# Performance work log

Measured on AMD Instinct MI355X. Metric: run time of the kernel, lower is better.

Reference implementation:

```python
import jax, jax.numpy as jnp
from jax import lax
import numpy as np

T, B, I, H, F, KEEP = 1000, 512, 64, 64, 128, 5
ALPHA = 20.0 / 100.0  # dt / tau


def setup_inputs() -> dict:
    key = jax.random.key(0)
    ks = jax.random.split(key, 9)
    s = 1.0 / np.sqrt(H)
    return {
        "x": jax.random.normal(ks[0], (T, B, I), jnp.float32),
        "h0": jnp.zeros((B, H), jnp.float32),
        "W_in": jax.random.normal(ks[1], (H, I), jnp.float32) * s,
        "b_in": jax.random.normal(ks[2], (H,), jnp.float32) * s,
        "W_hh": jax.random.normal(ks[3], (H, H), jnp.float32) * s,
        "b_hh": jax.random.normal(ks[4], (H,), jnp.float32) * s,
        "W1": jax.random.normal(ks[5], (F, KEEP * H), jnp.float32) / np.sqrt(KEEP * H),
        "b1": jax.random.normal(ks[6], (F,), jnp.float32) * 0.01,
        "W2": jax.random.normal(ks[7], (H, F), jnp.float32) / np.sqrt(F),
        "b2": jax.random.normal(ks[8], (H,), jnp.float32) * 0.01,
    }


def reference(x, h0, W_in, b_in, W_hh, b_hh, W1, b1, W2, b2):
    # CT-RNN with leaky integration; feedback via MLP on the last 5 hiddens
    # once 5 steps have accumulated. KC = 0.5*I, so the feedback mix is
    # h = 0.5*h_obs + 0.5*h_mlp.
    Tn, Bn, _ = x.shape
    Hn = h0.shape[1]
    buf0 = jnp.zeros((KEEP, Bn, Hn), x.dtype)  # oldest-first ring of hiddens

    def step(carry, inp):
        h, buf = carry
        xt, i = inp
        h_obs = jax.nn.relu(xt @ W_in.T + b_in + h @ W_hh.T + b_hh)
        h_obs = h * (1.0 - ALPHA) + h_obs * ALPHA
        # mlp feedback on concat of last 5 hiddens (oldest..newest) -> [B, 5H]
        mlp_in = buf.transpose(1, 0, 2).reshape(Bn, KEEP * Hn)
        h_mlp = jax.nn.relu(mlp_in @ W1.T + b1) @ W2.T + b2
        h_new = jnp.where(i >= KEEP, 0.5 * h_obs + 0.5 * h_mlp, h_obs)
        buf = jnp.concatenate([buf[1:], h_new[None]], axis=0)
        return (h_new, buf), h_new

    (hT, _), out = lax.scan(step, (h0, buf0), (x, jnp.arange(Tn)))
    return out, hT
```

## Files before the change

kernel.cpp:

```cpp
#include <hip/hip_runtime.h>

typedef short bf16x8 __attribute__((ext_vector_type(8)));
typedef float f32x4  __attribute__((ext_vector_type(4)));

#define TSTEPS 1000
#define BATCH  512
#define HID    64
#define INPD   64
#define FEAT   128
#define KEEP   5
#define KH     320
#define ALPHA  0.2f
#define BB     2
#define NBLK   (BATCH/BB)
#define NTHR   512

#define MFMA(a,b,c) __builtin_amdgcn_mfma_f32_16x16x32_bf16(a, b, c, 0, 0, 0)

template<int P> struct IC { static constexpr int v = P; };

__device__ __forceinline__ void barrier_fast() {
  asm volatile("s_waitcnt lgkmcnt(0)" ::: "memory");
  __builtin_amdgcn_s_barrier();
  asm volatile("" ::: "memory");
}

__device__ __forceinline__ f32x4 fold2(f32x4 v) {
  f32x4 r;
  r.x = v.x + __shfl_xor(v.x, 2);
  r.y = v.y + __shfl_xor(v.y, 2);
  r.z = v.z + __shfl_xor(v.z, 2);
  r.w = v.w + __shfl_xor(v.w, 2);
  return r;
}

__device__ __forceinline__ void pack4(float x0, float x1, float x2, float x3,
                                      unsigned &h0, unsigned &h1,
                                      unsigned &l0, unsigned &l1) {
  unsigned a0 = __float_as_uint(x0), a1 = __float_as_uint(x1);
  unsigned a2 = __float_as_uint(x2), a3 = __float_as_uint(x3);
  h0 = __builtin_amdgcn_perm(a1, a0, 0x07060302u);
  h1 = __builtin_amdgcn_perm(a3, a2, 0x07060302u);
  float r0 = x0 - __uint_as_float(a0 & 0xFFFF0000u);
  float r1 = x1 - __uint_as_float(a1 & 0xFFFF0000u);
  float r2 = x2 - __uint_as_float(a2 & 0xFFFF0000u);
  float r3 = x3 - __uint_as_float(a3 & 0xFFFF0000u);
  asm("v_cvt_pk_bf16_f32 %0, %1, %2" : "=v"(l0) : "v"(r0), "v"(r1));
  asm("v_cvt_pk_bf16_f32 %0, %1, %2" : "=v"(l1) : "v"(r2), "v"(r3));
}

__device__ __forceinline__ void pack_frag(float4 v0, float4 v1, bf16x8 &hi, bf16x8 &lo) {
  int4 h4, l4;
  pack4(v0.x, v0.y, v0.z, v0.w, (unsigned&)h4.x, (unsigned&)h4.y, (unsigned&)l4.x, (unsigned&)l4.y);
  pack4(v1.x, v1.y, v1.z, v1.w, (unsigned&)h4.z, (unsigned&)h4.w, (unsigned&)l4.z, (unsigned&)l4.w);
  hi = __builtin_bit_cast(bf16x8, h4);
  lo = __builtin_bit_cast(bf16x8, l4);
}

__device__ __forceinline__ void load_wfrag(const float* p, bf16x8 &hi, bf16x8 &lo) {
  float4 v0 = *(const float4*)p;
  float4 v1 = *(const float4*)(p + 4);
  pack_frag(v0, v1, hi, lo);
}

__global__ __launch_bounds__(NTHR, 2) void seq_kernel(
    const float* __restrict__ x,    float* __restrict__ io,
    const float* __restrict__ h0g,
    const float* __restrict__ W_in, const float* __restrict__ b_in,
    const float* __restrict__ W_hh, const float* __restrict__ b_hh,
    const float* __restrict__ W1,   const float* __restrict__ b1,
    const float* __restrict__ W2,   const float* __restrict__ b2) {

  __shared__ __align__(16) short B1lds[1024];
  __shared__ __align__(16) short a_s[512];
  __shared__ __align__(16) float xin_s[2][128];

  const int tid  = threadIdx.x;
  const int w    = tid >> 6;
  const int lane = tid & 63;
  const int q15  = lane & 15;
  const int g    = lane >> 4;
  const int b0   = blockIdx.x * BB;
  const bool gA  = (w < 4);
  const int r0c  = 16*(w & 3) + 4*g;
  const int f0   = 16*w + 4*g;
  const int c01  = q15 & 1;

  const int aWH = (w>>1)*128 + (2*(w&1) + (g>>1))*32 + q15*8 + 4*(g&1);
  const int aRD = g*32 + (q15 & 3)*8;
  const int bWH = ((w&3)>>1)*512 + ((2*(w&3) + (g>>1)) & 3)*128 + q15*8 + 4*(g&1);
  const int bRD = g*128 + q15*8;

  const f32x4 vz = {0.f, 0.f, 0.f, 0.f};
  const bf16x8 z8 = {0,0,0,0,0,0,0,0};

  bf16x8 w1h[10], w1l[10];
#pragma unroll
  for (int jt = 0; jt < 10; ++jt)
    load_wfrag(W1 + (size_t)(16*w + q15)*KH + jt*32 + 8*g, w1h[jt], w1l[jt]);

  bf16x8 wxh[6], wxl[6];
#pragma unroll
  for (int i = 0; i < 6; ++i) { wxh[i] = z8; wxl[i] = z8; }
  f32x4 biasv = vz, b2r = vz;
  f32x4 b1r = *(const f32x4*)(b1 + f0);
  if (gA) {
#pragma unroll
    for (int kt = 0; kt < 2; ++kt)
      load_wfrag(W_hh + (size_t)(16*w + q15)*HID + kt*32 + 8*g, wxh[kt], wxl[kt]);
#pragma unroll
    for (int kt = 0; kt < 4; ++kt)
      load_wfrag(W2 + (size_t)(16*w + q15)*FEAT + kt*32 + 8*g, wxh[2+kt], wxl[2+kt]);
    b2r = *(const f32x4*)(b2 + r0c);
  } else {
#pragma unroll
    for (int kt = 0; kt < 2; ++kt)
      load_wfrag(W_in + (size_t)(16*(w-4) + q15)*INPD + kt*32 + 8*g, wxh[kt], wxl[kt]);
    biasv = *(const f32x4*)(b_in + r0c) + *(const f32x4*)(b_hh + r0c);
  }

  for (int i = tid; i < 512; i += NTHR) ((unsigned*)B1lds)[i] = 0u;
  __syncthreads();

  f32x4 hprev = vz;
  float4 xc0, xc1, xc2, xc3;
  if (gA) {
    if (q15 < 2) {
      hprev = *(const f32x4*)(h0g + (size_t)(b0 + q15)*HID + r0c);
      unsigned n0, n1, n2, n3;
      pack4(hprev.x, hprev.y, hprev.z, hprev.w, n0, n1, n2, n3);
      *(uint2*)&B1lds[bWH]      = make_uint2(n0, n1);
      *(uint2*)&B1lds[bWH + 16] = make_uint2(n2, n3);
    }
  } else {
    const float* xp = x + (size_t)(b0 + c01)*INPD + 8*g;
    float4 v0 = *(const float4*)xp;        float4 v1 = *(const float4*)(xp + 4);
    float4 v2 = *(const float4*)(xp + 32); float4 v3 = *(const float4*)(xp + 36);
    bf16x8 th0, tl0, th1, tl1;
    pack_frag(v0, v1, th0, tl0);
    pack_frag(v2, v3, th1, tl1);
    bf16x8 f0b = (q15 & 2) ? tl0 : th0;
    bf16x8 f1b = (q15 & 2) ? tl1 : th1;
    f32x4 aH = vz, aL = vz;
    aH = MFMA(wxh[0], f0b, aH); aH = MFMA(wxh[1], f1b, aH);
    aL = MFMA(wxl[0], f0b, aL); aL = MFMA(wxl[1], f1b, aL);
    f32x4 xi = fold2(aH + aL) + biasv;
    if (q15 < 2) *(f32x4*)&xin_s[0][q15*64 + r0c] = xi;
    const float* xq = x + (size_t)1*BATCH*INPD + (size_t)(b0 + c01)*INPD + 8*g;
    xc0 = *(const float4*)xq;        xc1 = *(const float4*)(xq + 4);
    xc2 = *(const float4*)(xq + 32); xc3 = *(const float4*)(xq + 36);
  }

  bf16x8 rb[KEEP][2];
#pragma unroll
  for (int s = 0; s < KEEP; ++s) { rb[s][0] = z8; rb[s][1] = z8; }
  __syncthreads();

  int t5 = 0;
  auto step = [&](auto pc) {
    constexpr int ph = decltype(pc)::v;
    constexpr int sN = (ph + 4) % 5;
    const int t = t5 + ph;

    float4 xn0, xn1, xn2, xn3;
    if (!gA) {
      int tn = t + 2; if (tn > TSTEPS-1) tn = TSTEPS-1;
      const float* xp = x + (size_t)tn*BATCH*INPD + (size_t)(b0 + c01)*INPD + 8*g;
      xn0 = *(const float4*)xp;        xn1 = *(const float4*)(xp + 4);
      xn2 = *(const float4*)(xp + 32); xn3 = *(const float4*)(xp + 36);
    }

    rb[sN][0] = *(const bf16x8*)&B1lds[bRD];
    rb[sN][1] = *(const bf16x8*)&B1lds[bRD + 512];

    f32x4 aH = vz, aL = vz;
#pragma unroll
    for (int e = 1; e <= 5; ++e) {
      const int s = (sN + e) % 5;
      const int r = ((s - ph) % 5 + 5) % 5;
#pragma unroll
      for (int q = 0; q < 2; ++q) {
        const int jt = 2*r + q;
        aH = MFMA(w1h[jt], rb[s][q], aH);
        aL = MFMA(w1l[jt], rb[s][q], aL);
      }
    }
    {
      f32x4 apre = fold2(aH + aL) + b1r;
      f32x4 av = __builtin_elementwise_max(apre, vz);
      unsigned p0, p1, p2, p3;
      pack4(av.x, av.y, av.z, av.w, p0, p1, p2, p3);
      if (q15 < 2) {
        *(uint2*)&a_s[aWH]      = make_uint2(p0, p1);
        *(uint2*)&a_s[aWH + 16] = make_uint2(p2, p3);
      }
    }

    if (!gA) {
      bf16x8 th0, tl0, th1, tl1;
      pack_frag(xc0, xc1, th0, tl0);
      pack_frag(xc2, xc3, th1, tl1);
      bf16x8 f0b = (q15 & 2) ? tl0 : th0;
      bf16x8 f1b = (q15 & 2) ? tl1 : th1;
      f32x4 xH = vz, xL = vz;
      xH = MFMA(wxh[0], f0b, xH); xH = MFMA(wxh[1], f1b, xH);
      xL = MFMA(wxl[0], f0b, xL); xL = MFMA(wxl[1], f1b, xL);
      f32x4 xi = fold2(xH + xL) + biasv;
      if (q15 < 2) *(f32x4*)&xin_s[(t + 1) & 1][q15*64 + r0c] = xi;
      xc0 = xn0; xc1 = xn1; xc2 = xn2; xc3 = xn3;
    }
    barrier_fast();

    if (gA) {
      bf16x8 af0 = *(const bf16x8*)&a_s[aRD +   0];
      bf16x8 af1 = *(const bf16x8*)&a_s[aRD + 128];
      bf16x8 af2 = *(const bf16x8*)&a_s[aRD + 256];
      bf16x8 af3 = *(const bf16x8*)&a_s[aRD + 384];
      f32x4 xinv = *(const f32x4*)&xin_s[t & 1][(q15 & 1)*64 + r0c];
      f32x4 rH = vz, rL = vz;
      rH = MFMA(wxh[0], rb[sN][0], rH); rH = MFMA(wxh[1], rb[sN][1], rH);
      rL = MFMA(wxl[0], rb[sN][0], rL); rL = MFMA(wxl[1], rb[sN][1], rL);
      f32x4 mH = vz, mL = vz;
      mH = MFMA(wxh[2], af0, mH); mL = MFMA(wxl[2], af0, mL);
      mH = MFMA(wxh[3], af1, mH); mL = MFMA(wxl[3], af1, mL);
      mH = MFMA(wxh[4], af2, mH); mL = MFMA(wxl[4], af2, mL);
      mH = MFMA(wxh[5], af3, mH); mL = MFMA(wxl[5], af3, mL);
      f32x4 pre = fold2(rH + rL) + xinv;
      f32x4 rl_ = __builtin_elementwise_max(pre, vz);
      f32x4 hobs = hprev * (1.f - ALPHA) + rl_ * ALPHA;
      f32x4 hm = fold2(mH + mL) + b2r;
      f32x4 hn = (t >= KEEP) ? (hobs + hm) * 0.5f : hobs;
      if (q15 < 2) {
        *(f32x4*)(io + (size_t)t*BATCH*HID + (size_t)(b0 + q15)*HID + r0c) = hn;
        if (t == TSTEPS-1)
          *(f32x4*)(io + (size_t)TSTEPS*BATCH*HID + (size_t)(b0 + q15)*HID + r0c) = hn;
        unsigned n0, n1, n2, n3;
        pack4(hn.x, hn.y, hn.z, hn.w, n0, n1, n2, n3);
        *(uint2*)&B1lds[bWH]      = make_uint2(n0, n1);
        *(uint2*)&B1lds[bWH + 16] = make_uint2(n2, n3);
      }
      hprev = hn;
    }
    barrier_fast();
  };

  for (t5 = 0; t5 < TSTEPS; t5 += 5) {
    step(IC<0>{});
    step(IC<1>{});
    step(IC<2>{});
    step(IC<3>{});
    step(IC<4>{});
  }
}

extern "C" void kernel_launch(void* const* d_in, const int* in_sizes, int n_in,
                              void* d_out, int out_size, void* d_ws, size_t ws_size,
                              hipStream_t stream) {
  (void)in_sizes; (void)n_in; (void)out_size; (void)d_ws; (void)ws_size;
  const float* x    = (const float*)d_in[0];
  const float* h0   = (const float*)d_in[1];
  const float* W_in = (const float*)d_in[2];
  const float* b_in = (const float*)d_in[3];
  const float* W_hh = (const float*)d_in[4];
  const float* b_hh = (const float*)d_in[5];
  const float* W1   = (const float*)d_in[6];
  const float* b1   = (const float*)d_in[7];
  const float* W2   = (const float*)d_in[8];
  const float* b2   = (const float*)d_in[9];
  float* out = (float*)d_out;

  seq_kernel<<<NBLK, NTHR, 0, stream>>>(x, out, h0, W_in, b_in, W_hh, b_hh, W1, b1, W2, b2);
}
```

Before: 1.159 ms.

## Precompute older-history MLP partial sums in previous step off the critical path

```diff
diff --git a/kernel.cpp b/kernel.cpp
--- a/kernel.cpp
+++ b/kernel.cpp
@@ -141,10 +141,10 @@
     pack_frag(v2, v3, th1, tl1);
     bf16x8 f0b = (q15 & 2) ? tl0 : th0;
     bf16x8 f1b = (q15 & 2) ? tl1 : th1;
-    f32x4 aH = vz, aL = vz;
-    aH = MFMA(wxh[0], f0b, aH); aH = MFMA(wxh[1], f1b, aH);
-    aL = MFMA(wxl[0], f0b, aL); aL = MFMA(wxl[1], f1b, aL);
-    f32x4 xi = fold2(aH + aL) + biasv;
+    f32x4 aHx = vz, aLx = vz;
+    aHx = MFMA(wxh[0], f0b, aHx); aHx = MFMA(wxh[1], f1b, aHx);
+    aLx = MFMA(wxl[0], f0b, aLx); aLx = MFMA(wxl[1], f1b, aLx);
+    f32x4 xi = fold2(aHx + aLx) + biasv;
     if (q15 < 2) *(f32x4*)&xin_s[0][q15*64 + r0c] = xi;
     const float* xq = x + (size_t)1*BATCH*INPD + (size_t)(b0 + c01)*INPD + 8*g;
     xc0 = *(const float4*)xq;        xc1 = *(const float4*)(xq + 4);
@@ -154,6 +154,8 @@
   bf16x8 rb[KEEP][2];
 #pragma unroll
   for (int s = 0; s < KEEP; ++s) { rb[s][0] = z8; rb[s][1] = z8; }
+
+  f32x4 aH = vz, aL = vz;
   __syncthreads();
 
   int t5 = 0;
@@ -162,29 +164,13 @@
     constexpr int sN = (ph + 4) % 5;
     const int t = t5 + ph;
 
-    float4 xn0, xn1, xn2, xn3;
-    if (!gA) {
-      int tn = t + 2; if (tn > TSTEPS-1) tn = TSTEPS-1;
-      const float* xp = x + (size_t)tn*BATCH*INPD + (size_t)(b0 + c01)*INPD + 8*g;
-      xn0 = *(const float4*)xp;        xn1 = *(const float4*)(xp + 4);
-      xn2 = *(const float4*)(xp + 32); xn3 = *(const float4*)(xp + 36);
-    }
-
     rb[sN][0] = *(const bf16x8*)&B1lds[bRD];
     rb[sN][1] = *(const bf16x8*)&B1lds[bRD + 512];
 
-    f32x4 aH = vz, aL = vz;
-#pragma unroll
-    for (int e = 1; e <= 5; ++e) {
-      const int s = (sN + e) % 5;
-      const int r = ((s - ph) % 5 + 5) % 5;
-#pragma unroll
-      for (int q = 0; q < 2; ++q) {
-        const int jt = 2*r + q;
-        aH = MFMA(w1h[jt], rb[s][q], aH);
-        aL = MFMA(w1l[jt], rb[s][q], aL);
-      }
-    }
+    aH = MFMA(w1h[8], rb[sN][0], aH);
+    aL = MFMA(w1l[8], rb[sN][0], aL);
+    aH = MFMA(w1h[9], rb[sN][1], aH);
+    aL = MFMA(w1l[9], rb[sN][1], aL);
     {
       f32x4 apre = fold2(aH + aL) + b1r;
       f32x4 av = __builtin_elementwise_max(apre, vz);
@@ -195,28 +181,23 @@
         *(uint2*)&a_s[aWH + 16] = make_uint2(p2, p3);
       }
     }
-
-    if (!gA) {
-      bf16x8 th0, tl0, th1, tl1;
-      pack_frag(xc0, xc1, th0, tl0);
-      pack_frag(xc2, xc3, th1, tl1);
-      bf16x8 f0b = (q15 & 2) ? tl0 : th0;
-      bf16x8 f1b = (q15 & 2) ? tl1 : th1;
-      f32x4 xH = vz, xL = vz;
-      xH = MFMA(wxh[0], f0b, xH); xH = MFMA(wxh[1], f1b, xH);
-      xL = MFMA(wxl[0], f0b, xL); xL = MFMA(wxl[1], f1b, xL);
-      f32x4 xi = fold2(xH + xL) + biasv;
-      if (q15 < 2) *(f32x4*)&xin_s[(t + 1) & 1][q15*64 + r0c] = xi;
-      xc0 = xn0; xc1 = xn1; xc2 = xn2; xc3 = xn3;
-    }
     barrier_fast();
 
+    f32x4 nH = vz, nL = vz;
     if (gA) {
       bf16x8 af0 = *(const bf16x8*)&a_s[aRD +   0];
       bf16x8 af1 = *(const bf16x8*)&a_s[aRD + 128];
       bf16x8 af2 = *(const bf16x8*)&a_s[aRD + 256];
       bf16x8 af3 = *(const bf16x8*)&a_s[aRD + 384];
       f32x4 xinv = *(const f32x4*)&xin_s[t & 1][(q15 & 1)*64 + r0c];
+#pragma unroll
+      for (int r = 0; r < 4; ++r) {
+        const int s = (ph + 1 + r) % 5;
+        nH = MFMA(w1h[2*r],   rb[s][0], nH);
+        nH = MFMA(w1h[2*r+1], rb[s][1], nH);
+        nL = MFMA(w1l[2*r],   rb[s][0], nL);
+        nL = MFMA(w1l[2*r+1], rb[s][1], nL);
+      }
       f32x4 rH = vz, rL = vz;
       rH = MFMA(wxh[0], rb[sN][0], rH); rH = MFMA(wxh[1], rb[sN][1], rH);
       rL = MFMA(wxl[0], rb[sN][0], rL); rL = MFMA(wxl[1], rb[sN][1], rL);
@@ -240,7 +221,35 @@
         *(uint2*)&B1lds[bWH + 16] = make_uint2(n2, n3);
       }
       hprev = hn;
+    } else {
+      float4 xn0, xn1, xn2, xn3;
+      {
+        int tn = t + 2; if (tn > TSTEPS-1) tn = TSTEPS-1;
+        const float* xp = x + (size_t)tn*BATCH*INPD + (size_t)(b0 + c01)*INPD + 8*g;
+        xn0 = *(const float4*)xp;        xn1 = *(const float4*)(xp + 4);
+        xn2 = *(const float4*)(xp + 32); xn3 = *(const float4*)(xp + 36);
+      }
+#pragma unroll
+      for (int r = 0; r < 4; ++r) {
+        const int s = (ph + 1 + r) % 5;
+        nH = MFMA(w1h[2*r],   rb[s][0], nH);
+        nH = MFMA(w1h[2*r+1], rb[s][1], nH);
+        nL = MFMA(w1l[2*r],   rb[s][0], nL);
+        nL = MFMA(w1l[2*r+1], rb[s][1], nL);
+      }
+      bf16x8 th0, tl0, th1, tl1;
+      pack_frag(xc0, xc1, th0, tl0);
+      pack_frag(xc2, xc3, th1, tl1);
+      bf16x8 f0b = (q15 & 2) ? tl0 : th0;
+      bf16x8 f1b = (q15 & 2) ? tl1 : th1;
+      f32x4 xH = vz, xL = vz;
+      xH = MFMA(wxh[0], f0b, xH); xH = MFMA(wxh[1], f1b, xH);
+      xL = MFMA(wxl[0], f0b, xL); xL = MFMA(wxl[1], f1b, xL);
+      f32x4 xi = fold2(xH + xL) + biasv;
+      if (q15 < 2) *(f32x4*)&xin_s[(t + 1) & 1][q15*64 + r0c] = xi;
+      xc0 = xn0; xc1 = xn1; xc2 = xn2; xc3 = xn3;
     }
+    aH = nH; aL = nL;
     barrier_fast();
   };
 
```

Measured after the change: 974.3 us. 15.9% less time.
